# Kernel optimization log

Measured on AMD Instinct MI355X. Metric: run time of the kernel, lower is better.

Reference implementation:

```python
import jax, jax.numpy as jnp
import numpy as np

TEMP = 0.5
PATCH = 8
EPS = 1e-05


def _to_patches(x, h, w):
    # [B,C,H,W] -> [B*PATCH*PATCH, h*w, C], patch order (b, j, k) row-major
    B, C, H, W = x.shape
    x = x.reshape(B, C, PATCH, h, PATCH, w)
    x = x.transpose(0, 2, 4, 3, 5, 1)  # B, j, k, h, w, C
    return x.reshape(B * PATCH * PATCH, h * w, C)


def setup_inputs() -> dict:
    key = jax.random.key(0)
    k1, k2, k3, k4, k5 = jax.random.split(key, 5)
    B, C, H, W, L = 8, 256, 64, 64, 32
    return {
        "main_out": jax.random.normal(k1, (B, C, H, W), dtype=jnp.float32),
        "ema_out": jax.random.normal(k2, (B, C, H, W), dtype=jnp.float32),
        "main_label": jax.random.uniform(k3, (B, 4 * H, 4 * W), dtype=jnp.float32),
        "neg_banks": jax.random.normal(k4, (L, C, H // PATCH, W // PATCH), dtype=jnp.float32),
        "pos_banks": jax.random.normal(k5, (L, C, H // PATCH, W // PATCH), dtype=jnp.float32),
    }


def reference(main_out, ema_out, main_label, neg_banks, pos_banks):
    B, C, H, W = main_out.shape
    h, w = H // PATCH, W // PATCH
    hh, ww = 4 * h, 4 * w

    anchors = _to_patches(main_out, h, w)      # [BP, hw, C]
    pos_pair = _to_patches(ema_out, h, w)      # [BP, hw, C]

    neg_flat = neg_banks.transpose(0, 2, 3, 1).reshape(-1, C)  # [L*h*w, C]
    pos_flat = pos_banks.transpose(0, 2, 3, 1).reshape(-1, C)

    # per-patch mean of label, order (b, j, k) matching _to_patches
    lab = main_label.reshape(B, PATCH, hh, PATCH, ww).mean(axis=(2, 4))  # [B,8,8]
    use_pos = (lab.reshape(-1) < 0.1)[:, None, None]  # [BP,1,1]

    sim_neg = jnp.einsum("pnc,mc->pnm", anchors, neg_flat) / TEMP
    sim_posbank = jnp.einsum("pnc,mc->pnm", anchors, pos_flat) / TEMP
    neg_sim = jnp.where(use_pos, sim_posbank, sim_neg)  # [BP, hw, M]

    pos_sim = (anchors * pos_pair).sum(-1, keepdims=True) / TEMP  # [BP, hw, 1]

    allsim = jnp.concatenate([pos_sim, neg_sim], axis=-1)
    m = allsim.max(axis=-1, keepdims=True)
    denom = jnp.exp(allsim - m).sum(-1) + EPS            # [BP, hw]
    frac = jnp.exp(pos_sim - m)[..., 0] / denom
    loss_patch = -jnp.log(frac + EPS)                    # [BP, hw]
    # sum of per-patch means divided by B*PATCH^2 == global mean (equal patch sizes)
    return loss_patch.mean()
```

## Files before the change

### kernel.cpp

```cpp
#include <hip/hip_runtime.h>

typedef __attribute__((ext_vector_type(2))) long long2v;
typedef __attribute__((ext_vector_type(4))) float f32x4;

#define EPSV 1e-5f
#define SCALE 2.885390081777927f

__device__ __forceinline__ float fast_exp2(float x) { return __builtin_amdgcn_exp2f(x); }

__device__ __forceinline__ unsigned char f32_to_fp8(float f) {
  return (unsigned char)(__builtin_amdgcn_cvt_pk_fp8_f32(f, f, 0, false) & 0xff);
}


__global__ __launch_bounds__(256) void cpl_prep(
    const float* __restrict__ mainO, const float* __restrict__ emaO,
    const float* __restrict__ label, const float* __restrict__ negB,
    const float* __restrict__ posB,
    unsigned char* __restrict__ Apk, float* __restrict__ posDot,
    int* __restrict__ flags, unsigned char* __restrict__ bankN,
    unsigned char* __restrict__ bankP)
{
  __shared__ __align__(16) unsigned char shU[64 * 256];
  __shared__ float shF[4][64];
  const int bid = blockIdx.x;
  const int t = threadIdx.x;

  if (bid < 512) {
    const int b = bid >> 6, y = bid & 63;
    const int cg = t >> 4;
    const int x4 = t & 15;
    const float* mB = mainO + (((size_t)b * 256 + cg) * 64 + y) * 64 + x4 * 4;
    const float* eB = emaO  + (((size_t)b * 256 + cg) * 64 + y) * 64 + x4 * 4;
    float4 acc4 = make_float4(0.f, 0.f, 0.f, 0.f);
#pragma unroll
    for (int pass = 0; pass < 16; ++pass) {
      const int c = pass * 16 + cg;
      const float4 mv = *(const float4*)(mB + (size_t)pass * 16 * 4096);
      const float4 ev = *(const float4*)(eB + (size_t)pass * 16 * 4096);
      acc4.x += mv.x * ev.x; acc4.y += mv.y * ev.y;
      acc4.z += mv.z * ev.z; acc4.w += mv.w * ev.w;
      const float vals[4] = {mv.x, mv.y, mv.z, mv.w};
#pragma unroll
      for (int j = 0; j < 4; ++j) {
        const int x = x4 * 4 + j;
        shU[x * 256 + (c ^ ((x & 7) << 4))] = f32_to_fp8(vals[j]);
      }
    }
    acc4.x += __shfl_xor(acc4.x, 16, 64); acc4.y += __shfl_xor(acc4.y, 16, 64);
    acc4.z += __shfl_xor(acc4.z, 16, 64); acc4.w += __shfl_xor(acc4.w, 16, 64);
    acc4.x += __shfl_xor(acc4.x, 32, 64); acc4.y += __shfl_xor(acc4.y, 32, 64);
    acc4.z += __shfl_xor(acc4.z, 32, 64); acc4.w += __shfl_xor(acc4.w, 32, 64);
    if ((t & 63) < 16) *(float4*)&shF[t >> 6][(t & 15) * 4] = acc4;
    __syncthreads();
#pragma unroll
    for (int it = 0; it < 4; ++it) {
      const int lin = it * 256 + t;
      const int x = lin >> 4, c16 = lin & 15;
      const uint4 v = *(const uint4*)&shU[x * 256 + ((c16 * 16) ^ ((x & 7) << 4))];
      const int p = b * 64 + ((y >> 3) << 3) + (x >> 3);
      const int n = ((y & 7) << 3) + (x & 7);
      *(uint4*)&Apk[(size_t)p * 16384 + n * 256 + c16 * 16] = v;
    }
    if (t < 64) {
      const float pv = shF[0][t] + shF[1][t] + shF[2][t] + shF[3][t];
      const int p = b * 64 + ((y >> 3) << 3) + (t >> 3);
      const int n = ((y & 7) << 3) + (t & 7);
      posDot[p * 64 + n] = pv;
    }
  } else if (bid < 1024) {
    const int p = bid - 512;
    const int b = p >> 6, pj = (p >> 3) & 7, pk = p & 7;
    const size_t base = ((size_t)b * 256 + pj * 32) * 256 + pk * 32;
    float s = 0.f;
#pragma unroll
    for (int i = 0; i < 4; ++i) {
      const int e = t * 4 + i;
      s += label[base + (size_t)(e >> 5) * 256 + (e & 31)];
    }
#pragma unroll
    for (int d = 1; d < 64; d <<= 1) s += __shfl_xor(s, d, 64);
    if ((t & 63) == 0) shF[0][t >> 6] = s;
    __syncthreads();
    if (t == 0)
      flags[p] = ((shF[0][0] + shF[0][1] + shF[0][2] + shF[0][3]) * (1.f / 1024.f) < 0.1f) ? 1 : 0;
  } else {
    const int bb = bid - 1024;
    const float* src = (bb < 32 ? negB : posB) + (size_t)(bb & 31) * 16384;
    unsigned char* dst = (bb < 32 ? bankN : bankP) + (size_t)(bb & 31) * 16384;
#pragma unroll 8
    for (int it = 0; it < 64; ++it) {
      const int lin = it * 256 + t;
      const int c = lin >> 6, posi = lin & 63;
      shU[posi * 256 + (c ^ ((posi & 7) << 3))] = f32_to_fp8(src[lin] * SCALE);
    }
    __syncthreads();
#pragma unroll
    for (int it = 0; it < 4; ++it) {
      const int qK = (t >> 7) & 1, pair = (t >> 6) & 1;
      const int kg = (t >> 4) & 3, r16 = t & 15;
      const int posi = it * 16 + r16;
      const int kb = qK * 128 + pair * 64 + kg * 8;
      const int swz = (posi & 7) << 3;
      const unsigned long long lo = *(const unsigned long long*)&shU[posi * 256 + (kb ^ swz)];
      const unsigned long long hi = *(const unsigned long long*)&shU[posi * 256 + ((kb + 32) ^ swz)];
      long2v v; v[0] = (long)lo; v[1] = (long)hi;
      *(long2v*)(dst + it * 4096 + qK * 2048 + pair * 1024 + kg * 256 + r16 * 16) = v;
    }
  }
}

__global__ __launch_bounds__(256, 2) void cpl_main(
    const unsigned char* __restrict__ Apk, const float* __restrict__ posDot,
    const unsigned char* __restrict__ bankN, const unsigned char* __restrict__ bankP,
    const int* __restrict__ flags, float* __restrict__ blockSums)
{
  __shared__ float swS[4][64];

  const int p = blockIdx.x;
  const int t = threadIdx.x;
  const int l = t & 63, w = t >> 6;
  const int r16 = l & 15, kg = l >> 4;
  const int qph = (p * 22) & 63;

  const unsigned char* bankB = flags[p] ? bankP : bankN;
  const unsigned char* wsrc = bankB + (size_t)w * 131072;
  const int lofs = kg * 256 + r16 * 16;

  const unsigned char* Ab = Apk + (size_t)p * 16384;
  long long afrag[4][8];
#pragma unroll
  for (int mt = 0; mt < 4; ++mt)
#pragma unroll
    for (int ks = 0; ks < 8; ++ks)
      afrag[mt][ks] = *(const long long*)(Ab + (mt * 16 + r16) * 256 + ks * 32 + kg * 8);
#pragma unroll
  for (int mt = 0; mt < 4; ++mt)
#pragma unroll
    for (int ks = 0; ks < 8; ++ks)
      asm volatile("" : "+v"(afrag[mt][ks]));

  f32x4 negInit[4];
#pragma unroll
  for (int mt = 0; mt < 4; ++mt) {
    f32x4 v = *(const f32x4*)(posDot + (size_t)p * 64 + mt * 16 + kg * 4);
#pragma unroll
    for (int i = 0; i < 4; ++i) negInit[mt][i] = -v[i] * SCALE;
  }
#pragma unroll
  for (int mt = 0; mt < 4; ++mt) asm volatile("" : "+v"(negInit[mt]));

  float s[16];
#pragma unroll
  for (int e = 0; e < 16; ++e) s[e] = 0.f;

  f32x4 acc[4];
  long2v A0, A1, B0, B1, C0, C1, D0, D1, E0, E1, F0, F1, G0, G1, H0, H1;

#define GLOAD(P0, P1, QQ) do {                                                     \
    const unsigned char* g_ = wsrc + (size_t)((((QQ) + qph) & 63)) * 2048 + lofs;  \
    P0 = *(const long2v*)g_;                                                       \
    P1 = *(const long2v*)(g_ + 1024);                                              \
  } while (0)

#define MFMA16(P0, P1, HALF) do {                                                  \
    if ((HALF) == 0) {                                                             \
      _Pragma("unroll") for (int mt = 0; mt < 4; ++mt)                             \
        acc[mt] = __builtin_amdgcn_mfma_f32_16x16x32_fp8_fp8(afrag[mt][0], P0[0],  \
                      negInit[mt], 0, 0, 0);                                       \
      _Pragma("unroll") for (int mt = 0; mt < 4; ++mt)                             \
        acc[mt] = __builtin_amdgcn_mfma_f32_16x16x32_fp8_fp8(afrag[mt][1], P0[1],  \
                      acc[mt], 0, 0, 0);                                           \
      _Pragma("unroll") for (int mt = 0; mt < 4; ++mt)                             \
        acc[mt] = __builtin_amdgcn_mfma_f32_16x16x32_fp8_fp8(afrag[mt][2], P1[0],  \
                      acc[mt], 0, 0, 0);                                           \
      _Pragma("unroll") for (int mt = 0; mt < 4; ++mt)                             \
        acc[mt] = __builtin_amdgcn_mfma_f32_16x16x32_fp8_fp8(afrag[mt][3], P1[1],  \
                      acc[mt], 0, 0, 0);                                           \
    } else {                                                                       \
      _Pragma("unroll") for (int mt = 0; mt < 4; ++mt)                             \
        acc[mt] = __builtin_amdgcn_mfma_f32_16x16x32_fp8_fp8(afrag[mt][4], P0[0],  \
                      acc[mt], 0, 0, 0);                                           \
      _Pragma("unroll") for (int mt = 0; mt < 4; ++mt)                             \
        acc[mt] = __builtin_amdgcn_mfma_f32_16x16x32_fp8_fp8(afrag[mt][5], P0[1],  \
                      acc[mt], 0, 0, 0);                                           \
      _Pragma("unroll") for (int mt = 0; mt < 4; ++mt)                             \
        acc[mt] = __builtin_amdgcn_mfma_f32_16x16x32_fp8_fp8(afrag[mt][6], P1[0],  \
                      acc[mt], 0, 0, 0);                                           \
      _Pragma("unroll") for (int mt = 0; mt < 4; ++mt)                             \
        acc[mt] = __builtin_amdgcn_mfma_f32_16x16x32_fp8_fp8(afrag[mt][7], P1[1],  \
                      acc[mt], 0, 0, 0);                                           \
    } } while (0)

#define EXPACC() do {                                                              \
    _Pragma("unroll") for (int mt = 0; mt < 4; ++mt)                               \
      _Pragma("unroll") for (int i = 0; i < 4; ++i)                                \
        s[mt * 4 + i] += fast_exp2(acc[mt][i]); } while (0)

#define STEP(QQ, U0, U1, L0, L1, HALF, DO_LOAD, DO_EXP) do {                       \
    if (DO_LOAD) GLOAD(L0, L1, (QQ) + 7);                                          \
    __builtin_amdgcn_sched_barrier(0);                                             \
    __builtin_amdgcn_s_setprio(1);                                                 \
    MFMA16(U0, U1, HALF);                                                          \
    __builtin_amdgcn_s_setprio(0);                                                 \
    if (DO_EXP) EXPACC();                                                          \
    __builtin_amdgcn_sched_barrier(0);                                             \
  } while (0)

  GLOAD(A0, A1, 0); GLOAD(B0, B1, 1); GLOAD(C0, C1, 2); GLOAD(D0, D1, 3);
  GLOAD(E0, E1, 4); GLOAD(F0, F1, 5); GLOAD(G0, G1, 6);

  for (int g = 0; g < 7; ++g) {
    const int n0 = g * 8;
    STEP(n0 + 0, A0, A1, H0, H1, 0, 1, 0);
    STEP(n0 + 1, B0, B1, A0, A1, 1, 1, 1);
    STEP(n0 + 2, C0, C1, B0, B1, 0, 1, 0);
    STEP(n0 + 3, D0, D1, C0, C1, 1, 1, 1);
    STEP(n0 + 4, E0, E1, D0, D1, 0, 1, 0);
    STEP(n0 + 5, F0, F1, E0, E1, 1, 1, 1);
    STEP(n0 + 6, G0, G1, F0, F1, 0, 1, 0);
    STEP(n0 + 7, H0, H1, G0, G1, 1, 1, 1);
  }
  STEP(56, A0, A1, H0, H1, 0, 1, 0);
  STEP(57, B0, B1, A0, A1, 1, 0, 1);
  STEP(58, C0, C1, B0, B1, 0, 0, 0);
  STEP(59, D0, D1, C0, C1, 1, 0, 1);
  STEP(60, E0, E1, D0, D1, 0, 0, 0);
  STEP(61, F0, F1, E0, E1, 1, 0, 1);
  STEP(62, G0, G1, F0, F1, 0, 0, 0);
  STEP(63, H0, H1, G0, G1, 1, 0, 1);

#undef STEP
#undef EXPACC
#undef MFMA16
#undef GLOAD

#pragma unroll
  for (int d = 1; d < 16; d <<= 1)
#pragma unroll
    for (int e = 0; e < 16; ++e) s[e] += __shfl_xor(s[e], d, 64);
  if (r16 == 0) {
#pragma unroll
    for (int mt = 0; mt < 4; ++mt)
#pragma unroll
      for (int i = 0; i < 4; ++i)
        swS[w][mt * 16 + kg * 4 + i] = s[mt * 4 + i];
  }
  __syncthreads();

  if (t < 64) {
    const float S = 1.f + swS[0][t] + swS[1][t] + swS[2][t] + swS[3][t];
    float loss = -logf(1.f / S + EPSV);
#pragma unroll
    for (int d = 1; d < 64; d <<= 1) loss += __shfl_xor(loss, d, 64);
    if (t == 0) blockSums[p] = loss;
  }
}

__global__ void cpl_final(const float* __restrict__ blockSums, float* __restrict__ out) {
  const int t = threadIdx.x;
  float s = blockSums[t] + blockSums[t + 256];
#pragma unroll
  for (int d = 1; d < 64; d <<= 1) s += __shfl_xor(s, d, 64);
  __shared__ float ps[4];
  if ((t & 63) == 0) ps[t >> 6] = s;
  __syncthreads();
  if (t == 0) out[0] = (ps[0] + ps[1] + ps[2] + ps[3]) * (1.f / 32768.f);
}

extern "C" void kernel_launch(void* const* d_in, const int* in_sizes, int n_in,
                              void* d_out, int out_size, void* d_ws, size_t ws_size,
                              hipStream_t stream) {
  const float* mainO = (const float*)d_in[0];
  const float* emaO  = (const float*)d_in[1];
  const float* label = (const float*)d_in[2];
  const float* negB  = (const float*)d_in[3];
  const float* posB  = (const float*)d_in[4];
  float* out = (float*)d_out;

  char* ws = (char*)d_ws;
  float*         blockSums = (float*)ws;
  int*           flags     = (int*)(ws + 2048);
  unsigned char* bankN     = (unsigned char*)(ws + 4096);
  unsigned char* bankP     = (unsigned char*)(ws + 528384);
  float*         posDot    = (float*)(ws + 1052672);
  unsigned char* Apk       = (unsigned char*)(ws + 1183744);

  hipLaunchKernelGGL(cpl_prep, dim3(1088), dim3(256), 0, stream,
                     mainO, emaO, label, negB, posB, Apk, posDot, flags, bankN, bankP);
  hipLaunchKernelGGL(cpl_main, dim3(512), dim3(256), 0, stream,
                     Apk, posDot, bankN, bankP, flags, blockSums);
  hipLaunchKernelGGL(cpl_final, dim3(1), dim3(256), 0, stream, blockSums, out);
}
```

Before: 49.29 us.

## Process two patches per block to reuse bank fragments across anchors

Each block now handles two adjacent patches, so every bank tile loaded from global memory feeds MFMAs for both anchor sets. The grid is halved to 256 blocks and launch bounds drop to one block per SM. When the two patches need different banks, the block runs two passes and keeps only the matching half of each pass. The costs are doubled register use for A fragments and accumulators, lower occupancy, and redundant MFMA work whenever the two flags differ.

Measured after the change: 55.03 us. 1.12x slower.

```diff
diff --git a/kernel.cpp b/kernel.cpp
--- a/kernel.cpp
+++ b/kernel.cpp
@@ -110,150 +110,181 @@
   }
 }
 
-__global__ __launch_bounds__(256, 2) void cpl_main(
+__global__ __launch_bounds__(256, 1) void cpl_main(
     const unsigned char* __restrict__ Apk, const float* __restrict__ posDot,
     const unsigned char* __restrict__ bankN, const unsigned char* __restrict__ bankP,
     const int* __restrict__ flags, float* __restrict__ blockSums)
 {
-  __shared__ float swS[4][64];
-
-  const int p = blockIdx.x;
+  __shared__ float swS[2][4][64];
+
+  const int bid = blockIdx.x;
   const int t = threadIdx.x;
   const int l = t & 63, w = t >> 6;
   const int r16 = l & 15, kg = l >> 4;
-  const int qph = (p * 22) & 63;
-
-  const unsigned char* bankB = flags[p] ? bankP : bankN;
-  const unsigned char* wsrc = bankB + (size_t)w * 131072;
+  const int qph = (bid * 22) & 63;
+
+  const int p0 = bid * 2, p1 = bid * 2 + 1;
+  const int f0 = flags[p0], f1 = flags[p1];
+  const int npass = (f0 == f1) ? 1 : 2;
   const int lofs = kg * 256 + r16 * 16;
 
-  const unsigned char* Ab = Apk + (size_t)p * 16384;
-  long long afrag[4][8];
+  const unsigned char* Ab0 = Apk + (size_t)p0 * 16384;
+  const unsigned char* Ab1 = Apk + (size_t)p1 * 16384;
+  long long afrag0[4][8], afrag1[4][8];
 #pragma unroll
   for (int mt = 0; mt < 4; ++mt)
 #pragma unroll
-    for (int ks = 0; ks < 8; ++ks)
-      afrag[mt][ks] = *(const long long*)(Ab + (mt * 16 + r16) * 256 + ks * 32 + kg * 8);
+    for (int ks = 0; ks < 8; ++ks) {
+      const int off = (mt * 16 + r16) * 256 + ks * 32 + kg * 8;
+      afrag0[mt][ks] = *(const long long*)(Ab0 + off);
+      afrag1[mt][ks] = *(const long long*)(Ab1 + off);
+    }
 #pragma unroll
   for (int mt = 0; mt < 4; ++mt)
 #pragma unroll
-    for (int ks = 0; ks < 8; ++ks)
-      asm volatile("" : "+v"(afrag[mt][ks]));
-
-  f32x4 negInit[4];
+    for (int ks = 0; ks < 8; ++ks) {
+      asm volatile("" : "+v"(afrag0[mt][ks]));
+      asm volatile("" : "+v"(afrag1[mt][ks]));
+    }
+
+  f32x4 negInit0[4], negInit1[4];
 #pragma unroll
   for (int mt = 0; mt < 4; ++mt) {
-    f32x4 v = *(const f32x4*)(posDot + (size_t)p * 64 + mt * 16 + kg * 4);
-#pragma unroll
-    for (int i = 0; i < 4; ++i) negInit[mt][i] = -v[i] * SCALE;
-  }
-#pragma unroll
-  for (int mt = 0; mt < 4; ++mt) asm volatile("" : "+v"(negInit[mt]));
-
-  float s[16];
-#pragma unroll
-  for (int e = 0; e < 16; ++e) s[e] = 0.f;
-
-  f32x4 acc[4];
-  long2v A0, A1, B0, B1, C0, C1, D0, D1, E0, E1, F0, F1, G0, G1, H0, H1;
+    f32x4 v0 = *(const f32x4*)(posDot + (size_t)p0 * 64 + mt * 16 + kg * 4);
+    f32x4 v1 = *(const f32x4*)(posDot + (size_t)p1 * 64 + mt * 16 + kg * 4);
+#pragma unroll
+    for (int i = 0; i < 4; ++i) {
+      negInit0[mt][i] = -v0[i] * SCALE;
+      negInit1[mt][i] = -v1[i] * SCALE;
+    }
+  }
+#pragma unroll
+  for (int mt = 0; mt < 4; ++mt) {
+    asm volatile("" : "+v"(negInit0[mt]));
+    asm volatile("" : "+v"(negInit1[mt]));
+  }
 
 #define GLOAD(P0, P1, QQ) do {                                                     \
-    const unsigned char* g_ = wsrc + (size_t)((((QQ) + qph) & 63)) * 2048 + lofs;  \
+    const unsigned char* g_ = wsrc + (size_t)((((QQ) + qph) & 63)) * 2048;         \
     P0 = *(const long2v*)g_;                                                       \
     P1 = *(const long2v*)(g_ + 1024);                                              \
   } while (0)
 
-#define MFMA16(P0, P1, HALF) do {                                                  \
+#define MFMA16_P(AF, ACC, NI, P0, P1, HALF) do {                                   \
     if ((HALF) == 0) {                                                             \
       _Pragma("unroll") for (int mt = 0; mt < 4; ++mt)                             \
-        acc[mt] = __builtin_amdgcn_mfma_f32_16x16x32_fp8_fp8(afrag[mt][0], P0[0],  \
-                      negInit[mt], 0, 0, 0);                                       \
-      _Pragma("unroll") for (int mt = 0; mt < 4; ++mt)                             \
-        acc[mt] = __builtin_amdgcn_mfma_f32_16x16x32_fp8_fp8(afrag[mt][1], P0[1],  \
-                      acc[mt], 0, 0, 0);                                           \
-      _Pragma("unroll") for (int mt = 0; mt < 4; ++mt)                             \
-        acc[mt] = __builtin_amdgcn_mfma_f32_16x16x32_fp8_fp8(afrag[mt][2], P1[0],  \
-                      acc[mt], 0, 0, 0);                                           \
-      _Pragma("unroll") for (int mt = 0; mt < 4; ++mt)                             \
-        acc[mt] = __builtin_amdgcn_mfma_f32_16x16x32_fp8_fp8(afrag[mt][3], P1[1],  \
-                      acc[mt], 0, 0, 0);                                           \
+        ACC[mt] = __builtin_amdgcn_mfma_f32_16x16x32_fp8_fp8(AF[mt][0], P0[0],     \
+                      NI[mt], 0, 0, 0);                                            \
+      _Pragma("unroll") for (int mt = 0; mt < 4; ++mt)                             \
+        ACC[mt] = __builtin_amdgcn_mfma_f32_16x16x32_fp8_fp8(AF[mt][1], P0[1],     \
+                      ACC[mt], 0, 0, 0);                                           \
+      _Pragma("unroll") for (int mt = 0; mt < 4; ++mt)                             \
+        ACC[mt] = __builtin_amdgcn_mfma_f32_16x16x32_fp8_fp8(AF[mt][2], P1[0],     \
+                      ACC[mt], 0, 0, 0);                                           \
+      _Pragma("unroll") for (int mt = 0; mt < 4; ++mt)                             \
+        ACC[mt] = __builtin_amdgcn_mfma_f32_16x16x32_fp8_fp8(AF[mt][3], P1[1],     \
+                      ACC[mt], 0, 0, 0);                                           \
     } else {                                                                       \
       _Pragma("unroll") for (int mt = 0; mt < 4; ++mt)                             \
-        acc[mt] = __builtin_amdgcn_mfma_f32_16x16x32_fp8_fp8(afrag[mt][4], P0[0],  \
-                      acc[mt], 0, 0, 0);                                           \
-      _Pragma("unroll") for (int mt = 0; mt < 4; ++mt)                             \
-        acc[mt] = __builtin_amdgcn_mfma_f32_16x16x32_fp8_fp8(afrag[mt][5], P0[1],  \
-                      acc[mt], 0, 0, 0);                                           \
-      _Pragma("unroll") for (int mt = 0; mt < 4; ++mt)                             \
-        acc[mt] = __builtin_amdgcn_mfma_f32_16x16x32_fp8_fp8(afrag[mt][6], P1[0],  \
-                      acc[mt], 0, 0, 0);                                           \
-      _Pragma("unroll") for (int mt = 0; mt < 4; ++mt)                             \
-        acc[mt] = __builtin_amdgcn_mfma_f32_16x16x32_fp8_fp8(afrag[mt][7], P1[1],  \
-                      acc[mt], 0, 0, 0);                                           \
+        ACC[mt] = __builtin_amdgcn_mfma_f32_16x16x32_fp8_fp8(AF[mt][4], P0[0],     \
+                      ACC[mt], 0, 0, 0);                                           \
+      _Pragma("unroll") for (int mt = 0; mt < 4; ++mt)                             \
+        ACC[mt] = __builtin_amdgcn_mfma_f32_16x16x32_fp8_fp8(AF[mt][5], P0[1],     \
+                      ACC[mt], 0, 0, 0);                                           \
+      _Pragma("unroll") for (int mt = 0; mt < 4; ++mt)                             \
+        ACC[mt] = __builtin_amdgcn_mfma_f32_16x16x32_fp8_fp8(AF[mt][6], P1[0],     \
+                      ACC[mt], 0, 0, 0);                                           \
+      _Pragma("unroll") for (int mt = 0; mt < 4; ++mt)                             \
+        ACC[mt] = __builtin_amdgcn_mfma_f32_16x16x32_fp8_fp8(AF[mt][7], P1[1],     \
+                      ACC[mt], 0, 0, 0);                                           \
     } } while (0)
 
-#define EXPACC() do {                                                              \
+#define EXPACC(ACC, S) do {                                                        \
     _Pragma("unroll") for (int mt = 0; mt < 4; ++mt)                               \
       _Pragma("unroll") for (int i = 0; i < 4; ++i)                                \
-        s[mt * 4 + i] += fast_exp2(acc[mt][i]); } while (0)
+        S[mt * 4 + i] += fast_exp2(ACC[mt][i]); } while (0)
 
 #define STEP(QQ, U0, U1, L0, L1, HALF, DO_LOAD, DO_EXP) do {                       \
     if (DO_LOAD) GLOAD(L0, L1, (QQ) + 7);                                          \
     __builtin_amdgcn_sched_barrier(0);                                             \
     __builtin_amdgcn_s_setprio(1);                                                 \
-    MFMA16(U0, U1, HALF);                                                          \
+    MFMA16_P(afrag0, acc0, negInit0, U0, U1, HALF);                                \
+    MFMA16_P(afrag1, acc1, negInit1, U0, U1, HALF);                                \
     __builtin_amdgcn_s_setprio(0);                                                 \
-    if (DO_EXP) EXPACC();                                                          \
+    if (DO_EXP) { EXPACC(acc0, s0); EXPACC(acc1, s1); }                            \
     __builtin_amdgcn_sched_barrier(0);                                             \
   } while (0)
 
-  GLOAD(A0, A1, 0); GLOAD(B0, B1, 1); GLOAD(C0, C1, 2); GLOAD(D0, D1, 3);
-  GLOAD(E0, E1, 4); GLOAD(F0, F1, 5); GLOAD(G0, G1, 6);
-
-  for (int g = 0; g < 7; ++g) {
-    const int n0 = g * 8;
-    STEP(n0 + 0, A0, A1, H0, H1, 0, 1, 0);
-    STEP(n0 + 1, B0, B1, A0, A1, 1, 1, 1);
-    STEP(n0 + 2, C0, C1, B0, B1, 0, 1, 0);
-    STEP(n0 + 3, D0, D1, C0, C1, 1, 1, 1);
-    STEP(n0 + 4, E0, E1, D0, D1, 0, 1, 0);
-    STEP(n0 + 5, F0, F1, E0, E1, 1, 1, 1);
-    STEP(n0 + 6, G0, G1, F0, F1, 0, 1, 0);
-    STEP(n0 + 7, H0, H1, G0, G1, 1, 1, 1);
-  }
-  STEP(56, A0, A1, H0, H1, 0, 1, 0);
-  STEP(57, B0, B1, A0, A1, 1, 0, 1);
-  STEP(58, C0, C1, B0, B1, 0, 0, 0);
-  STEP(59, D0, D1, C0, C1, 1, 0, 1);
-  STEP(60, E0, E1, D0, D1, 0, 0, 0);
-  STEP(61, F0, F1, E0, E1, 1, 0, 1);
-  STEP(62, G0, G1, F0, F1, 0, 0, 0);
-  STEP(63, H0, H1, G0, G1, 1, 0, 1);
+  for (int pass = 0; pass < npass; ++pass) {
+    const int fUse = (pass == 0) ? f0 : f1;
+    const unsigned char* wsrc = (fUse ? bankP : bankN) + (size_t)w * 131072 + lofs;
+
+    float s0[16], s1[16];
+#pragma unroll
+    for (int e = 0; e < 16; ++e) { s0[e] = 0.f; s1[e] = 0.f; }
+
+    f32x4 acc0[4], acc1[4];
+    long2v A0, A1, B0, B1, C0, C1, D0, D1, E0, E1, F0, F1, G0, G1, H0, H1;
+
+    GLOAD(A0, A1, 0); GLOAD(B0, B1, 1); GLOAD(C0, C1, 2); GLOAD(D0, D1, 3);
+    GLOAD(E0, E1, 4); GLOAD(F0, F1, 5); GLOAD(G0, G1, 6);
+
+    for (int g = 0; g < 7; ++g) {
+      const int n0 = g * 8;
+      STEP(n0 + 0, A0, A1, H0, H1, 0, 1, 0);
+      STEP(n0 + 1, B0, B1, A0, A1, 1, 1, 1);
+      STEP(n0 + 2, C0, C1, B0, B1, 0, 1, 0);
+      STEP(n0 + 3, D0, D1, C0, C1, 1, 1, 1);
+      STEP(n0 + 4, E0, E1, D0, D1, 0, 1, 0);
+      STEP(n0 + 5, F0, F1, E0, E1, 1, 1, 1);
+      STEP(n0 + 6, G0, G1, F0, F1, 0, 1, 0);
+      STEP(n0 + 7, H0, H1, G0, G1, 1, 1, 1);
+    }
+    STEP(56, A0, A1, H0, H1, 0, 1, 0);
+    STEP(57, B0, B1, A0, A1, 1, 0, 1);
+    STEP(58, C0, C1, B0, B1, 0, 0, 0);
+    STEP(59, D0, D1, C0, C1, 1, 0, 1);
+    STEP(60, E0, E1, D0, D1, 0, 0, 0);
+    STEP(61, F0, F1, E0, E1, 1, 0, 1);
+    STEP(62, G0, G1, F0, F1, 0, 0, 0);
+    STEP(63, H0, H1, G0, G1, 1, 0, 1);
+
+#pragma unroll
+    for (int d = 1; d < 16; d <<= 1)
+#pragma unroll
+      for (int e = 0; e < 16; ++e) {
+        s0[e] += __shfl_xor(s0[e], d, 64);
+        s1[e] += __shfl_xor(s1[e], d, 64);
+      }
+    if (r16 == 0) {
+      const bool keep0 = (npass == 1) || (pass == 0);
+      const bool keep1 = (npass == 1) || (pass == 1);
+#pragma unroll
+      for (int mt = 0; mt < 4; ++mt)
+#pragma unroll
+        for (int i = 0; i < 4; ++i) {
+          const int row = mt * 16 + kg * 4 + i;
+          if (keep0) swS[0][w][row] = s0[mt * 4 + i];
+          if (keep1) swS[1][w][row] = s1[mt * 4 + i];
+        }
+    }
+  }
 
 #undef STEP
 #undef EXPACC
-#undef MFMA16
+#undef MFMA16_P
 #undef GLOAD
 
-#pragma unroll
-  for (int d = 1; d < 16; d <<= 1)
-#pragma unroll
-    for (int e = 0; e < 16; ++e) s[e] += __shfl_xor(s[e], d, 64);
-  if (r16 == 0) {
-#pragma unroll
-    for (int mt = 0; mt < 4; ++mt)
-#pragma unroll
-      for (int i = 0; i < 4; ++i)
-        swS[w][mt * 16 + kg * 4 + i] = s[mt * 4 + i];
-  }
   __syncthreads();
 
-  if (t < 64) {
-    const float S = 1.f + swS[0][t] + swS[1][t] + swS[2][t] + swS[3][t];
+  if (t < 128) {
+    const int q2 = t >> 6, row = t & 63;
+    const float S = 1.f + swS[q2][0][row] + swS[q2][1][row]
+                        + swS[q2][2][row] + swS[q2][3][row];
     float loss = -logf(1.f / S + EPSV);
 #pragma unroll
     for (int d = 1; d < 64; d <<= 1) loss += __shfl_xor(loss, d, 64);
-    if (t == 0) blockSums[p] = loss;
+    if (row == 0) blockSums[bid * 2 + q2] = loss;
   }
 }
 
@@ -288,7 +319,7 @@
 
   hipLaunchKernelGGL(cpl_prep, dim3(1088), dim3(256), 0, stream,
                      mainO, emaO, label, negB, posB, Apk, posDot, flags, bankN, bankP);
-  hipLaunchKernelGGL(cpl_main, dim3(512), dim3(256), 0, stream,
+  hipLaunchKernelGGL(cpl_main, dim3(256), dim3(256), 0, stream,
                      Apk, posDot, bankN, bankP, flags, blockSums);
   hipLaunchKernelGGL(cpl_final, dim3(1), dim3(256), 0, stream, blockSums, out);
 }
```

## Stream bank tiles via global_load_lds DMA ring instead of register prefetch

Applied to the files above, without the earlier changes.

Replaces the 8-deep register-based prefetch of bank B-fragments with direct global-to-LDS loads into a per-wave 8-slot ring buffer. Reads come back from LDS just before each MFMA group, and explicit vmcnt waits track readiness. The goal is to free many VGPRs held by in-flight prefetch registers and to let the async DMA path overlap memory with MFMA. In exchange it adds 64KB of LDS per block, which may limit occupancy at 2 blocks per CU, plus extra LDS read latency per step.

New measurement: 53.01 us. 1.08x slower.

```diff
diff --git a/kernel.cpp b/kernel.cpp
--- a/kernel.cpp
+++ b/kernel.cpp
@@ -10,6 +10,12 @@
 
 __device__ __forceinline__ unsigned char f32_to_fp8(float f) {
   return (unsigned char)(__builtin_amdgcn_cvt_pk_fp8_f32(f, f, 0, false) & 0xff);
+}
+
+__device__ __forceinline__ void dma16(const void* g, void* l) {
+  __builtin_amdgcn_global_load_lds(
+      (const __attribute__((address_space(1))) unsigned*)g,
+      (__attribute__((address_space(3))) unsigned*)l, 16, 0, 0);
 }
 
 
@@ -115,6 +121,7 @@
     const unsigned char* __restrict__ bankN, const unsigned char* __restrict__ bankP,
     const int* __restrict__ flags, float* __restrict__ blockSums)
 {
+  __shared__ __align__(1024) unsigned char Bsm[4 * 8 * 2048];
   __shared__ float swS[4][64];
 
   const int p = blockIdx.x;
@@ -125,7 +132,8 @@
 
   const unsigned char* bankB = flags[p] ? bankP : bankN;
   const unsigned char* wsrc = bankB + (size_t)w * 131072;
-  const int lofs = kg * 256 + r16 * 16;
+  unsigned char* wlds = Bsm + w * 16384;
+  const int dmaOfs = l * 16;
 
   const unsigned char* Ab = Apk + (size_t)p * 16384;
   long long afrag[4][8];
@@ -150,18 +158,21 @@
 #pragma unroll
   for (int mt = 0; mt < 4; ++mt) asm volatile("" : "+v"(negInit[mt]));
 
+  asm volatile("s_waitcnt vmcnt(0)" ::: "memory");
+
+#define ISSUEQ(QQ, SLOT) do {                                                      \
+    const unsigned char* g_ = wsrc + (size_t)((((QQ) + qph) & 63)) * 2048 + dmaOfs;\
+    unsigned char* l_ = wlds + (SLOT) * 2048;                                      \
+    dma16(g_, l_);                                                                 \
+    dma16(g_ + 1024, l_ + 1024);                                                   \
+  } while (0)
+
   float s[16];
 #pragma unroll
   for (int e = 0; e < 16; ++e) s[e] = 0.f;
 
   f32x4 acc[4];
-  long2v A0, A1, B0, B1, C0, C1, D0, D1, E0, E1, F0, F1, G0, G1, H0, H1;
-
-#define GLOAD(P0, P1, QQ) do {                                                     \
-    const unsigned char* g_ = wsrc + (size_t)((((QQ) + qph) & 63)) * 2048 + lofs;  \
-    P0 = *(const long2v*)g_;                                                       \
-    P1 = *(const long2v*)(g_ + 1024);                                              \
-  } while (0)
+  const unsigned char* rbase = wlds + kg * 256 + r16 * 16;
 
 #define MFMA16(P0, P1, HALF) do {                                                  \
     if ((HALF) == 0) {                                                             \
@@ -197,43 +208,47 @@
       _Pragma("unroll") for (int i = 0; i < 4; ++i)                                \
         s[mt * 4 + i] += fast_exp2(acc[mt][i]); } while (0)
 
-#define STEP(QQ, U0, U1, L0, L1, HALF, DO_LOAD, DO_EXP) do {                       \
-    if (DO_LOAD) GLOAD(L0, L1, (QQ) + 7);                                          \
+#define STEP(QQ, SLOT, HALF, DO_ISSUE, WN, DO_EXP) do {                            \
+    asm volatile("s_waitcnt vmcnt(" #WN ")" ::: "memory");                         \
     __builtin_amdgcn_sched_barrier(0);                                             \
-    __builtin_amdgcn_s_setprio(1);                                                 \
-    MFMA16(U0, U1, HALF);                                                          \
-    __builtin_amdgcn_s_setprio(0);                                                 \
+    if (DO_ISSUE) ISSUEQ((QQ) + 7, ((SLOT) + 7) & 7);                              \
+    { const unsigned char* rb_ = rbase + (SLOT) * 2048;                            \
+      long2v P0 = *(const long2v*)rb_;                                             \
+      long2v P1 = *(const long2v*)(rb_ + 1024);                                    \
+      __builtin_amdgcn_s_setprio(1);                                               \
+      MFMA16(P0, P1, HALF);                                                        \
+      __builtin_amdgcn_s_setprio(0); }                                             \
     if (DO_EXP) EXPACC();                                                          \
     __builtin_amdgcn_sched_barrier(0);                                             \
   } while (0)
 
-  GLOAD(A0, A1, 0); GLOAD(B0, B1, 1); GLOAD(C0, C1, 2); GLOAD(D0, D1, 3);
-  GLOAD(E0, E1, 4); GLOAD(F0, F1, 5); GLOAD(G0, G1, 6);
+  ISSUEQ(0, 0); ISSUEQ(1, 1); ISSUEQ(2, 2); ISSUEQ(3, 3);
+  ISSUEQ(4, 4); ISSUEQ(5, 5); ISSUEQ(6, 6);
 
   for (int g = 0; g < 7; ++g) {
     const int n0 = g * 8;
-    STEP(n0 + 0, A0, A1, H0, H1, 0, 1, 0);
-    STEP(n0 + 1, B0, B1, A0, A1, 1, 1, 1);
-    STEP(n0 + 2, C0, C1, B0, B1, 0, 1, 0);
-    STEP(n0 + 3, D0, D1, C0, C1, 1, 1, 1);
-    STEP(n0 + 4, E0, E1, D0, D1, 0, 1, 0);
-    STEP(n0 + 5, F0, F1, E0, E1, 1, 1, 1);
-    STEP(n0 + 6, G0, G1, F0, F1, 0, 1, 0);
-    STEP(n0 + 7, H0, H1, G0, G1, 1, 1, 1);
-  }
-  STEP(56, A0, A1, H0, H1, 0, 1, 0);
-  STEP(57, B0, B1, A0, A1, 1, 0, 1);
-  STEP(58, C0, C1, B0, B1, 0, 0, 0);
-  STEP(59, D0, D1, C0, C1, 1, 0, 1);
-  STEP(60, E0, E1, D0, D1, 0, 0, 0);
-  STEP(61, F0, F1, E0, E1, 1, 0, 1);
-  STEP(62, G0, G1, F0, F1, 0, 0, 0);
-  STEP(63, H0, H1, G0, G1, 1, 0, 1);
+    STEP(n0 + 0, 0, 0, 1, 12, 0);
+    STEP(n0 + 1, 1, 1, 1, 12, 1);
+    STEP(n0 + 2, 2, 0, 1, 12, 0);
+    STEP(n0 + 3, 3, 1, 1, 12, 1);
+    STEP(n0 + 4, 4, 0, 1, 12, 0);
+    STEP(n0 + 5, 5, 1, 1, 12, 1);
+    STEP(n0 + 6, 6, 0, 1, 12, 0);
+    STEP(n0 + 7, 7, 1, 1, 12, 1);
+  }
+  STEP(56, 0, 0, 1, 12, 0);
+  STEP(57, 1, 1, 0, 12, 1);
+  STEP(58, 2, 0, 0, 10, 0);
+  STEP(59, 3, 1, 0,  8, 1);
+  STEP(60, 4, 0, 0,  6, 0);
+  STEP(61, 5, 1, 0,  4, 1);
+  STEP(62, 6, 0, 0,  2, 0);
+  STEP(63, 7, 1, 0,  0, 1);
 
 #undef STEP
 #undef EXPACC
 #undef MFMA16
-#undef GLOAD
+#undef ISSUEQ
 
 #pragma unroll
   for (int d = 1; d < 16; d <<= 1)
```

## Quantize negative/positive banks to FP4 and use scaled 16x16x128 mixed-precision MFMA

Applied to the files above, without the earlier changes.

Bank tensors are now quantized to 4-bit e2m1 instead of fp8, halving bank bytes. The anchor operand stays fp8 but is pre-scaled and repacked for the 16x16x128 scaled MFMA with fp8 A and fp4 B. This cuts MFMA instruction count and bank load traffic. It also makes the exp accumulation run every tile. The cost is a large accuracy loss: bank values are rounded to 8 magnitude levels, which can drift the loss away from the reference.

After: 64.07 us. 1.3x slower.

```diff
diff --git a/kernel.cpp b/kernel.cpp
--- a/kernel.cpp
+++ b/kernel.cpp
@@ -2,6 +2,8 @@
 
 typedef __attribute__((ext_vector_type(2))) long long2v;
 typedef __attribute__((ext_vector_type(4))) float f32x4;
+typedef __attribute__((ext_vector_type(4))) int i32x4;
+typedef __attribute__((ext_vector_type(8))) int i32x8;
 
 #define EPSV 1e-5f
 #define SCALE 2.885390081777927f
@@ -10,6 +12,21 @@
 
 __device__ __forceinline__ unsigned char f32_to_fp8(float f) {
   return (unsigned char)(__builtin_amdgcn_cvt_pk_fp8_f32(f, f, 0, false) & 0xff);
+}
+
+__device__ __forceinline__ unsigned f32_to_fp4(float v) {
+  const float m = fabsf(v);
+  unsigned c = (unsigned)(m > 0.25f) + (unsigned)(m > 0.75f) + (unsigned)(m > 1.25f)
+             + (unsigned)(m > 1.75f) + (unsigned)(m > 2.5f)  + (unsigned)(m > 3.5f)
+             + (unsigned)(m > 5.0f);
+  return c | (v < 0.f ? 8u : 0u);
+}
+
+__device__ __forceinline__ i32x8 expand4(long2v p) {
+  union { long2v l; i32x4 i; } u; u.l = p;
+  i32x8 r; r[0] = u.i[0]; r[1] = u.i[1]; r[2] = u.i[2]; r[3] = u.i[3];
+  r[4] = 0; r[5] = 0; r[6] = 0; r[7] = 0;
+  return r;
 }
 
 
@@ -44,7 +61,7 @@
 #pragma unroll
       for (int j = 0; j < 4; ++j) {
         const int x = x4 * 4 + j;
-        shU[x * 256 + (c ^ ((x & 7) << 4))] = f32_to_fp8(vals[j]);
+        shU[x * 256 + (c ^ ((x & 7) << 4))] = f32_to_fp8(vals[j] * SCALE);
       }
     }
     acc4.x += __shfl_xor(acc4.x, 16, 64); acc4.y += __shfl_xor(acc4.y, 16, 64);
@@ -55,12 +72,16 @@
     __syncthreads();
 #pragma unroll
     for (int it = 0; it < 4; ++it) {
-      const int lin = it * 256 + t;
-      const int x = lin >> 4, c16 = lin & 15;
-      const uint4 v = *(const uint4*)&shU[x * 256 + ((c16 * 16) ^ ((x & 7) << 4))];
+      const int id = it * 256 + t;
+      const int x = id >> 4, rem = id & 15;
+      const int kq = rem >> 3, kb = (rem >> 1) & 3, half = rem & 1;
+      const int cb = kq * 128 + kb * 32 + half * 16;
+      const uint4 v = *(const uint4*)&shU[x * 256 + (cb ^ ((x & 7) << 4))];
       const int p = b * 64 + ((y >> 3) << 3) + (x >> 3);
       const int n = ((y & 7) << 3) + (x & 7);
-      *(uint4*)&Apk[(size_t)p * 16384 + n * 256 + c16 * 16] = v;
+      const int mt = n >> 4, r16n = n & 15;
+      *(uint4*)&Apk[(size_t)p * 16384 + mt * 4096 + kq * 2048 + kb * 512 +
+                    r16n * 32 + half * 16] = v;
     }
     if (t < 64) {
       const float pv = shF[0][t] + shF[1][t] + shF[2][t] + shF[3][t];
@@ -87,25 +108,36 @@
   } else {
     const int bb = bid - 1024;
     const float* src = (bb < 32 ? negB : posB) + (size_t)(bb & 31) * 16384;
-    unsigned char* dst = (bb < 32 ? bankN : bankP) + (size_t)(bb & 31) * 16384;
+    unsigned char* dst = (bb < 32 ? bankN : bankP) + (size_t)(bb & 31) * 8192;
 #pragma unroll 8
     for (int it = 0; it < 64; ++it) {
       const int lin = it * 256 + t;
       const int c = lin >> 6, posi = lin & 63;
-      shU[posi * 256 + (c ^ ((posi & 7) << 3))] = f32_to_fp8(src[lin] * SCALE);
+      shU[posi * 256 + (c ^ ((posi & 7) << 3))] = (unsigned char)f32_to_fp4(src[lin]);
     }
     __syncthreads();
 #pragma unroll
-    for (int it = 0; it < 4; ++it) {
-      const int qK = (t >> 7) & 1, pair = (t >> 6) & 1;
-      const int kg = (t >> 4) & 3, r16 = t & 15;
-      const int posi = it * 16 + r16;
-      const int kb = qK * 128 + pair * 64 + kg * 8;
+    for (int it = 0; it < 2; ++it) {
+      const int ch = it * 256 + t;
+      const int ct = ch >> 7, kq = (ch >> 6) & 1, kb = (ch >> 4) & 3, col = ch & 15;
+      const int posi = ct * 16 + col;
       const int swz = (posi & 7) << 3;
-      const unsigned long long lo = *(const unsigned long long*)&shU[posi * 256 + (kb ^ swz)];
-      const unsigned long long hi = *(const unsigned long long*)&shU[posi * 256 + ((kb + 32) ^ swz)];
-      long2v v; v[0] = (long)lo; v[1] = (long)hi;
-      *(long2v*)(dst + it * 4096 + qK * 2048 + pair * 1024 + kg * 256 + r16 * 16) = v;
+      const int cb = kq * 128 + kb * 32;
+      unsigned wrd[4];
+#pragma unroll
+      for (int w4 = 0; w4 < 4; ++w4) {
+        unsigned v = 0;
+#pragma unroll
+        for (int k = 0; k < 4; ++k) {
+          const int bo = w4 * 4 + k;
+          const unsigned lo = shU[posi * 256 + ((cb + 2 * bo) ^ swz)];
+          const unsigned hi = shU[posi * 256 + ((cb + 2 * bo + 1) ^ swz)];
+          v |= ((lo | (hi << 4)) & 0xffu) << (8 * k);
+        }
+        wrd[w4] = v;
+      }
+      uint4 o; o.x = wrd[0]; o.y = wrd[1]; o.z = wrd[2]; o.w = wrd[3];
+      *(uint4*)&dst[ct * 2048 + kq * 1024 + kb * 256 + col * 16] = o;
     }
   }
 }
@@ -121,24 +153,24 @@
   const int t = threadIdx.x;
   const int l = t & 63, w = t >> 6;
   const int r16 = l & 15, kg = l >> 4;
-  const int qph = (p * 22) & 63;
+  const int qph = (p * 11) & 31;
 
   const unsigned char* bankB = flags[p] ? bankP : bankN;
-  const unsigned char* wsrc = bankB + (size_t)w * 131072;
-  const int lofs = kg * 256 + r16 * 16;
+  const unsigned char* wsrc = bankB + (size_t)w * 65536;
+  const int lofs = l * 16;
 
   const unsigned char* Ab = Apk + (size_t)p * 16384;
-  long long afrag[4][8];
+  i32x8 afrag[4][2];
 #pragma unroll
   for (int mt = 0; mt < 4; ++mt)
 #pragma unroll
-    for (int ks = 0; ks < 8; ++ks)
-      afrag[mt][ks] = *(const long long*)(Ab + (mt * 16 + r16) * 256 + ks * 32 + kg * 8);
+    for (int kq = 0; kq < 2; ++kq)
+      afrag[mt][kq] = *(const i32x8*)(Ab + mt * 4096 + kq * 2048 + kg * 512 + r16 * 32);
 #pragma unroll
   for (int mt = 0; mt < 4; ++mt)
 #pragma unroll
-    for (int ks = 0; ks < 8; ++ks)
-      asm volatile("" : "+v"(afrag[mt][ks]));
+    for (int kq = 0; kq < 2; ++kq)
+      asm volatile("" : "+v"(afrag[mt][kq]));
 
   f32x4 negInit[4];
 #pragma unroll
@@ -157,82 +189,63 @@
   f32x4 acc[4];
   long2v A0, A1, B0, B1, C0, C1, D0, D1, E0, E1, F0, F1, G0, G1, H0, H1;
 
-#define GLOAD(P0, P1, QQ) do {                                                     \
-    const unsigned char* g_ = wsrc + (size_t)((((QQ) + qph) & 63)) * 2048 + lofs;  \
+#define GLOAD(P0, P1, TT) do {                                                     \
+    const unsigned char* g_ = wsrc + (size_t)((((TT) + qph) & 31)) * 2048 + lofs;  \
     P0 = *(const long2v*)g_;                                                       \
     P1 = *(const long2v*)(g_ + 1024);                                              \
   } while (0)
 
-#define MFMA16(P0, P1, HALF) do {                                                  \
-    if ((HALF) == 0) {                                                             \
-      _Pragma("unroll") for (int mt = 0; mt < 4; ++mt)                             \
-        acc[mt] = __builtin_amdgcn_mfma_f32_16x16x32_fp8_fp8(afrag[mt][0], P0[0],  \
-                      negInit[mt], 0, 0, 0);                                       \
-      _Pragma("unroll") for (int mt = 0; mt < 4; ++mt)                             \
-        acc[mt] = __builtin_amdgcn_mfma_f32_16x16x32_fp8_fp8(afrag[mt][1], P0[1],  \
-                      acc[mt], 0, 0, 0);                                           \
-      _Pragma("unroll") for (int mt = 0; mt < 4; ++mt)                             \
-        acc[mt] = __builtin_amdgcn_mfma_f32_16x16x32_fp8_fp8(afrag[mt][2], P1[0],  \
-                      acc[mt], 0, 0, 0);                                           \
-      _Pragma("unroll") for (int mt = 0; mt < 4; ++mt)                             \
-        acc[mt] = __builtin_amdgcn_mfma_f32_16x16x32_fp8_fp8(afrag[mt][3], P1[1],  \
-                      acc[mt], 0, 0, 0);                                           \
-    } else {                                                                       \
-      _Pragma("unroll") for (int mt = 0; mt < 4; ++mt)                             \
-        acc[mt] = __builtin_amdgcn_mfma_f32_16x16x32_fp8_fp8(afrag[mt][4], P0[0],  \
-                      acc[mt], 0, 0, 0);                                           \
-      _Pragma("unroll") for (int mt = 0; mt < 4; ++mt)                             \
-        acc[mt] = __builtin_amdgcn_mfma_f32_16x16x32_fp8_fp8(afrag[mt][5], P0[1],  \
-                      acc[mt], 0, 0, 0);                                           \
-      _Pragma("unroll") for (int mt = 0; mt < 4; ++mt)                             \
-        acc[mt] = __builtin_amdgcn_mfma_f32_16x16x32_fp8_fp8(afrag[mt][6], P1[0],  \
-                      acc[mt], 0, 0, 0);                                           \
-      _Pragma("unroll") for (int mt = 0; mt < 4; ++mt)                             \
-        acc[mt] = __builtin_amdgcn_mfma_f32_16x16x32_fp8_fp8(afrag[mt][7], P1[1],  \
-                      acc[mt], 0, 0, 0);                                           \
-    } } while (0)
+#define MFMA_TILE(P0, P1) do {                                                     \
+    i32x8 b8_ = expand4(P0);                                                       \
+    _Pragma("unroll") for (int mt = 0; mt < 4; ++mt)                               \
+      acc[mt] = __builtin_amdgcn_mfma_scale_f32_16x16x128_f8f6f4(                  \
+          afrag[mt][0], b8_, negInit[mt], 0, 4, 0, 127, 0, 127);                   \
+    b8_ = expand4(P1);                                                             \
+    _Pragma("unroll") for (int mt = 0; mt < 4; ++mt)                               \
+      acc[mt] = __builtin_amdgcn_mfma_scale_f32_16x16x128_f8f6f4(                  \
+          afrag[mt][1], b8_, acc[mt], 0, 4, 0, 127, 0, 127);                       \
+  } while (0)
 
 #define EXPACC() do {                                                              \
     _Pragma("unroll") for (int mt = 0; mt < 4; ++mt)                               \
       _Pragma("unroll") for (int i = 0; i < 4; ++i)                                \
         s[mt * 4 + i] += fast_exp2(acc[mt][i]); } while (0)
 
-#define STEP(QQ, U0, U1, L0, L1, HALF, DO_LOAD, DO_EXP) do {                       \
-    if (DO_LOAD) GLOAD(L0, L1, (QQ) + 7);                                          \
+#define STEP(TT, U0, U1, L0, L1, DO_LOAD) do {                                     \
+    if (DO_LOAD) GLOAD(L0, L1, (TT) + 7);                                          \
     __builtin_amdgcn_sched_barrier(0);                                             \
     __builtin_amdgcn_s_setprio(1);                                                 \
-    MFMA16(U0, U1, HALF);                                                          \
+    MFMA_TILE(U0, U1);                                                             \
     __builtin_amdgcn_s_setprio(0);                                                 \
-    if (DO_EXP) EXPACC();                                                          \
+    EXPACC();                                                                      \
     __builtin_amdgcn_sched_barrier(0);                                             \
   } while (0)
 
   GLOAD(A0, A1, 0); GLOAD(B0, B1, 1); GLOAD(C0, C1, 2); GLOAD(D0, D1, 3);
   GLOAD(E0, E1, 4); GLOAD(F0, F1, 5); GLOAD(G0, G1, 6);
 
-  for (int g = 0; g < 7; ++g) {
-    const int n0 = g * 8;
-    STEP(n0 + 0, A0, A1, H0, H1, 0, 1, 0);
-    STEP(n0 + 1, B0, B1, A0, A1, 1, 1, 1);
-    STEP(n0 + 2, C0, C1, B0, B1, 0, 1, 0);
-    STEP(n0 + 3, D0, D1, C0, C1, 1, 1, 1);
-    STEP(n0 + 4, E0, E1, D0, D1, 0, 1, 0);
-    STEP(n0 + 5, F0, F1, E0, E1, 1, 1, 1);
-    STEP(n0 + 6, G0, G1, F0, F1, 0, 1, 0);
-    STEP(n0 + 7, H0, H1, G0, G1, 1, 1, 1);
-  }
-  STEP(56, A0, A1, H0, H1, 0, 1, 0);
-  STEP(57, B0, B1, A0, A1, 1, 0, 1);
-  STEP(58, C0, C1, B0, B1, 0, 0, 0);
-  STEP(59, D0, D1, C0, C1, 1, 0, 1);
-  STEP(60, E0, E1, D0, D1, 0, 0, 0);
-  STEP(61, F0, F1, E0, E1, 1, 0, 1);
-  STEP(62, G0, G1, F0, F1, 0, 0, 0);
-  STEP(63, H0, H1, G0, G1, 1, 0, 1);
+  for (int g = 0; g < 3; ++g) {
+    STEP(8 * g + 0, A0, A1, H0, H1, 1);
+    STEP(8 * g + 1, B0, B1, A0, A1, 1);
+    STEP(8 * g + 2, C0, C1, B0, B1, 1);
+    STEP(8 * g + 3, D0, D1, C0, C1, 1);
+    STEP(8 * g + 4, E0, E1, D0, D1, 1);
+    STEP(8 * g + 5, F0, F1, E0, E1, 1);
+    STEP(8 * g + 6, G0, G1, F0, F1, 1);
+    STEP(8 * g + 7, H0, H1, G0, G1, 1);
+  }
+  STEP(24, A0, A1, H0, H1, 1);
+  STEP(25, B0, B1, A0, A1, 0);
+  STEP(26, C0, C1, B0, B1, 0);
+  STEP(27, D0, D1, C0, C1, 0);
+  STEP(28, E0, E1, D0, D1, 0);
+  STEP(29, F0, F1, E0, E1, 0);
+  STEP(30, G0, G1, F0, F1, 0);
+  STEP(31, H0, H1, G0, G1, 0);
 
 #undef STEP
 #undef EXPACC
-#undef MFMA16
+#undef MFMA_TILE
 #undef GLOAD
 
 #pragma unroll
@@ -282,9 +295,9 @@
   float*         blockSums = (float*)ws;
   int*           flags     = (int*)(ws + 2048);
   unsigned char* bankN     = (unsigned char*)(ws + 4096);
-  unsigned char* bankP     = (unsigned char*)(ws + 528384);
-  float*         posDot    = (float*)(ws + 1052672);
-  unsigned char* Apk       = (unsigned char*)(ws + 1183744);
+  unsigned char* bankP     = (unsigned char*)(ws + 266240);
+  float*         posDot    = (float*)(ws + 528384);
+  unsigned char* Apk       = (unsigned char*)(ws + 659456);
 
   hipLaunchKernelGGL(cpl_prep, dim3(1088), dim3(256), 0, stream,
                      mainO, emaO, label, negB, posB, Apk, posDot, flags, bankN, bankP);
```
